# Performance work log

Hardware: AMD Instinct MI355X
Metric: run time of the kernel (lower is better)

## Reference

```python
import jax, jax.numpy as jnp
from jax import lax
import numpy as np

B, N, NPOINT, NSAMPLE, C = 4, 8192, 2048, 32, 128
RADIUS = 0.2
H1, H2, OUT = 64, 128, 128  # mlp: (3+C)->H1->H2, sas: H2->OUT


def fps(xyz, npoint):
    # furthest point sampling: xyz (B,N,3) -> idx (B,npoint) int32
    b, n, _ = xyz.shape
    init_idx = jnp.zeros((b,), jnp.int32)

    def step(carry, _):
        dist, last = carry
        p = jnp.take_along_axis(xyz, last[:, None, None], axis=1)  # (B,1,3)
        d = jnp.sum((xyz - p) ** 2, axis=-1)                       # (B,N)
        dist = jnp.minimum(dist, d)
        nxt = jnp.argmax(dist, axis=-1).astype(jnp.int32)
        return (dist, nxt), nxt

    (_, _), rest = lax.scan(step, (jnp.full((b, n), 1e10, jnp.float32), init_idx),
                            None, length=npoint - 1)
    return jnp.concatenate([init_idx[None, :], rest], axis=0).T    # (B,npoint)


def ball_query(xyz, new_xyz, radius, nsample):
    # xyz (B,N,3), new_xyz (B,S,3) -> idx (B,S,nsample) int32
    n = xyz.shape[1]
    d2 = jnp.sum((new_xyz[:, :, None, :] - xyz[:, None, :, :]) ** 2, axis=-1)  # (B,S,N)
    ar = jnp.arange(n, dtype=jnp.int32)
    keys = jnp.where(d2 <= radius * radius, ar, n)  # valid -> own index, invalid -> N
    neg_vals, _ = lax.top_k(-keys, nsample)          # smallest nsample keys
    idx = -neg_vals
    first = idx[..., :1]
    return jnp.where(idx >= n, first, idx)           # pad invalid with first valid


def gather_points(pts, idx):
    # pts (B,N,D), idx (B,S,ns) -> (B,S,ns,D)
    b, s, ns = idx.shape
    flat = jnp.take_along_axis(pts, idx.reshape(b, s * ns, 1), axis=1)
    return flat.reshape(b, s, ns, -1)


def setup_inputs() -> dict:
    key = jax.random.key(0)
    ks = jax.random.split(key, 8)
    xyz = jax.random.uniform(ks[0], (B, N, 3), dtype=jnp.float32)
    features = jax.random.normal(ks[1], (B, C, N), dtype=jnp.float32)
    cin = C + 3
    W1 = jax.random.normal(ks[2], (H1, cin), dtype=jnp.float32) / np.sqrt(cin)
    b1 = jnp.zeros((H1,), jnp.float32)
    W2 = jax.random.normal(ks[3], (H2, H1), dtype=jnp.float32) / np.sqrt(H1)
    b2 = jnp.zeros((H2,), jnp.float32)
    Wsa = jax.random.normal(ks[4], (OUT, H2), dtype=jnp.float32) / np.sqrt(H2)
    bsa = jnp.zeros((OUT,), jnp.float32)
    return {"xyz": xyz, "features": features, "W1": W1, "b1": b1,
            "W2": W2, "b2": b2, "Wsa": Wsa, "bsa": bsa}


def reference(xyz, features, W1, b1, W2, b2, Wsa, bsa):
    center_idx = fps(xyz, NPOINT)                                   # (B,S)
    new_xyz = jnp.take_along_axis(xyz, center_idx[:, :, None], axis=1)  # (B,S,3)
    g_idx = ball_query(xyz, new_xyz, RADIUS, NSAMPLE)               # (B,S,ns)
    g_xyz = gather_points(xyz, g_idx) - new_xyz[:, :, None, :]      # (B,S,ns,3) relative coords
    g_feat = gather_points(features.transpose(0, 2, 1), g_idx)      # (B,S,ns,C)
    h = jnp.concatenate([g_xyz, g_feat], axis=-1)                   # (B,S,ns,3+C)
    h = jax.nn.relu(jnp.einsum('bsnc,oc->bsno', h, W1) + b1)        # shared 1x1-conv MLP
    h = jax.nn.relu(jnp.einsum('bsnc,oc->bsno', h, W2) + b2)
    pooled = jnp.max(h, axis=2)                                     # max over nsample -> (B,S,H2)
    out = jnp.einsum('bsc,oc->bso', pooled, Wsa) + bsa              # sas channel mixer
    return new_xyz, out.transpose(0, 2, 1)                          # (B,S,3), (B,OUT,S)
```

## Files before the change

kernel.cpp:

```cpp
#include <hip/hip_runtime.h>
#include <cstdint>
#include <cstddef>

#define NB 4
#define NN 8192
#define NPTS 2048
#define NSAMP 32
#define NC 128
#define CIN 131
#define NH1 64
#define NH2 128
#define NOUTC 128
#define GCELLS 4096

typedef float v2f __attribute__((ext_vector_type(2)));
typedef unsigned long long ull;

__device__ __forceinline__ float d2_exact(float ax, float ay, float az,
                                          float bx, float by, float bz) {
  float dx = ax - bx, dy = ay - by, dz = az - bz;
  return __fadd_rn(__fadd_rn(__fmul_rn(dx, dx), __fmul_rn(dy, dy)),
                   __fmul_rn(dz, dz));
}

#if __has_builtin(__builtin_amdgcn_mov_dpp)
template <int CTRL>
__device__ __forceinline__ float dppf(float v) {
  return __int_as_float(
      __builtin_amdgcn_mov_dpp(__float_as_int(v), CTRL, 0xF, 0xF, true));
}
template <int CTRL>
__device__ __forceinline__ int dppi(int v) {
  return __builtin_amdgcn_mov_dpp(v, CTRL, 0xF, 0xF, true);
}
#else
template <int CTRL>
__device__ __forceinline__ float dppf(float v) {
  const int m = (CTRL == 0xB1) ? 1 : (CTRL == 0x4E) ? 2 : (CTRL == 0x141) ? 7 : 15;
  return __shfl_xor(v, m);
}
template <int CTRL>
__device__ __forceinline__ int dppi(int v) {
  const int m = (CTRL == 0xB1) ? 1 : (CTRL == 0x4E) ? 2 : (CTRL == 0x141) ? 7 : 15;
  return __shfl_xor(v, m);
}
#endif

template <int CTRL>
__device__ __forceinline__ ull dppk(ull k) {
  int hi = dppi<CTRL>((int)(k >> 32));
  int lo = dppi<CTRL>((int)(unsigned)k);
  return ((ull)(unsigned)hi << 32) | (unsigned)lo;
}
__device__ __forceinline__ ull shflk(ull k, int m) {
  int hi = __shfl_xor((int)(k >> 32), m);
  int lo = __shfl_xor((int)(unsigned)k, m);
  return ((ull)(unsigned)hi << 32) | (unsigned)lo;
}

template <int CTRL>
__device__ __forceinline__ void redk5(ull& k, float& x, float& y, float& z) {
  ull ok = dppk<CTRL>(k);
  float ox = dppf<CTRL>(x), oy = dppf<CTRL>(y), oz = dppf<CTRL>(z);
  bool t = ok > k;
  k = t ? ok : k;
  x = t ? ox : x;
  y = t ? oy : y;
  z = t ? oz : z;
}

__device__ __forceinline__ void red_pair(float& bv, int& bi, float ov, int oi) {
  bool t = (ov > bv) || (ov == bv && oi < bi);
  bv = t ? ov : bv;
  bi = t ? oi : bi;
}

#define SEL8V(A, kk, out)                     \
  {                                           \
    v2f t0_ = ((kk) & 2) ? A[1] : A[0];       \
    v2f t1_ = ((kk) & 2) ? A[3] : A[2];       \
    v2f t2_ = ((kk) & 4) ? t1_ : t0_;         \
    out = ((kk) & 1) ? t2_.y : t2_.x;         \
  }

__device__ __forceinline__ int spread3(int v) {
  return (v & 1) | ((v & 2) << 2) | ((v & 4) << 4) | ((v & 8) << 6);
}

__global__ __launch_bounds__(1024, 1) void sort_kernel(
    const float* __restrict__ xyz, float* __restrict__ xs,
    float* __restrict__ ys, float* __restrict__ zs, int* __restrict__ io) {
  __shared__ int hist[GCELLS];
  __shared__ int cbase[GCELLS];
  __shared__ int wtot[16];
  __shared__ int woff[16];
  const int b = blockIdx.x;
  const int tid = threadIdx.x;
  const int lane = tid & 63;
  const int wid = tid >> 6;
  const float* xb = xyz + (size_t)b * NN * 3;
  for (int i = tid; i < GCELLS; i += 1024) hist[i] = 0;
  __syncthreads();
  int cell[8];
  float px[8], py[8], pz[8];
#pragma unroll
  for (int k = 0; k < 8; ++k) {
    int j = tid + (k << 10);
    float x = xb[j * 3 + 0], y = xb[j * 3 + 1], z = xb[j * 3 + 2];
    px[k] = x; py[k] = y; pz[k] = z;
    int cx = min(15, max(0, (int)(x * 16.0f)));
    int cy = min(15, max(0, (int)(y * 16.0f)));
    int cz = min(15, max(0, (int)(z * 16.0f)));
    cell[k] = spread3(cx) | (spread3(cy) << 1) | (spread3(cz) << 2);
    atomicAdd(&hist[cell[k]], 1);
  }
  __syncthreads();
  const int i0 = tid * 4;
  int h0 = hist[i0], h1 = hist[i0 + 1], h2 = hist[i0 + 2], h3 = hist[i0 + 3];
  int s4 = h0 + h1 + h2 + h3;
  int v = s4;
#pragma unroll
  for (int d = 1; d < 64; d <<= 1) {
    int o = __shfl_up(v, d);
    if (lane >= d) v += o;
  }
  if (lane == 63) wtot[wid] = v;
  __syncthreads();
  if (tid < 16) {
    int acc = 0;
    for (int w = 0; w < 16; ++w) {
      if (w == tid) woff[tid] = acc;
      acc += wtot[w];
    }
  }
  __syncthreads();
  int eb = woff[wid] + v - s4;
  cbase[i0] = eb;
  cbase[i0 + 1] = eb + h0;
  cbase[i0 + 2] = eb + h0 + h1;
  cbase[i0 + 3] = eb + h0 + h1 + h2;
  __syncthreads();
  for (int i = tid; i < GCELLS; i += 1024) hist[i] = 0;
  __syncthreads();
  const size_t bo = (size_t)b * NN;
#pragma unroll
  for (int k = 0; k < 8; ++k) {
    int pos = cbase[cell[k]] + atomicAdd(&hist[cell[k]], 1);
    xs[bo + pos] = px[k];
    ys[bo + pos] = py[k];
    zs[bo + pos] = pz[k];
    io[bo + pos] = tid + (k << 10);
  }
}

__global__ __launch_bounds__(1024, 1) void fps_kernel(
    const float* __restrict__ xyz, const float* __restrict__ xs,
    const float* __restrict__ ys, const float* __restrict__ zs,
    const int* __restrict__ io, float* __restrict__ newxyz) {
#pragma clang fp contract(off)
  const int b = blockIdx.x;
  const int tid = threadIdx.x;
  const int lane = tid & 63;
  const int wid = tid >> 6;
  const size_t bo = (size_t)b * NN;

  v2f X2[4], Y2[4], Z2[4], D2[4];
  unsigned invI[8];
#pragma unroll
  for (int p = 0; p < 4; ++p) {
    int s0 = tid * 8 + 2 * p, s1 = s0 + 1;
    X2[p].x = xs[bo + s0]; X2[p].y = xs[bo + s1];
    Y2[p].x = ys[bo + s0]; Y2[p].y = ys[bo + s1];
    Z2[p].x = zs[bo + s0]; Z2[p].y = zs[bo + s1];
    invI[2 * p] = ~(unsigned)io[bo + s0];
    invI[2 * p + 1] = ~(unsigned)io[bo + s1];
    D2[p].x = 1e30f;
    D2[p].y = 1e30f;
  }

  __shared__ int skh[2][16], skl[2][16];
  __shared__ float sx[2][16], sy[2][16], sz[2][16];

  const float* xb = xyz + (size_t)b * NN * 3;
  float cx = xb[0], cy = xb[1], cz = xb[2];
  if (tid == 0) {
    newxyz[(size_t)b * NPTS * 3 + 0] = cx;
    newxyz[(size_t)b * NPTS * 3 + 1] = cy;
    newxyz[(size_t)b * NPTS * 3 + 2] = cz;
  }

  for (int t = 1; t < NPTS; ++t) {
    const int par = t & 1;
    const v2f cxv = {cx, cx}, cyv = {cy, cy}, czv = {cz, cz};
    ull bkey = 0ull;
    int kw = 0;
#pragma unroll
    for (int p = 0; p < 4; ++p) {
      v2f dx = X2[p] - cxv;
      v2f dy = Y2[p] - cyv;
      v2f dz = Z2[p] - czv;
      v2f s = dx * dx + dy * dy + dz * dz;
      v2f nd;
      nd.x = fminf(D2[p].x, s.x);
      nd.y = fminf(D2[p].y, s.y);
      D2[p] = nd;
      ull k0 = ((ull)__float_as_uint(nd.x) << 32) | invI[2 * p];
      bool c0 = k0 > bkey;
      bkey = c0 ? k0 : bkey;
      kw = c0 ? (2 * p) : kw;
      ull k1 = ((ull)__float_as_uint(nd.y) << 32) | invI[2 * p + 1];
      bool c1 = k1 > bkey;
      bkey = c1 ? k1 : bkey;
      kw = c1 ? (2 * p + 1) : kw;
    }
    ull rk = bkey;
    { ull o = dppk<0xB1>(rk);  rk = o > rk ? o : rk; }
    { ull o = dppk<0x4E>(rk);  rk = o > rk ? o : rk; }
    { ull o = dppk<0x141>(rk); rk = o > rk ? o : rk; }
    { ull o = dppk<0x140>(rk); rk = o > rk ? o : rk; }
    { ull o = shflk(rk, 16);   rk = o > rk ? o : rk; }
    { ull o = shflk(rk, 32);   rk = o > rk ? o : rk; }
    if (bkey == rk) {
      float ox, oy, oz;
      SEL8V(X2, kw, ox);
      SEL8V(Y2, kw, oy);
      SEL8V(Z2, kw, oz);
      skh[par][wid] = (int)(rk >> 32);
      skl[par][wid] = (int)(unsigned)rk;
      sx[par][wid] = ox;
      sy[par][wid] = oy;
      sz[par][wid] = oz;
    }
    __syncthreads();
    const int sl = lane & 15;
    ull mk = ((ull)(unsigned)skh[par][sl] << 32) | (unsigned)skl[par][sl];
    float xx = sx[par][sl], yy = sy[par][sl], zz = sz[par][sl];
    redk5<0xB1>(mk, xx, yy, zz);
    redk5<0x4E>(mk, xx, yy, zz);
    redk5<0x141>(mk, xx, yy, zz);
    redk5<0x140>(mk, xx, yy, zz);
    cx = xx;
    cy = yy;
    cz = zz;
    if (tid == 0) {
      size_t o = ((size_t)b * NPTS + t) * 3;
      newxyz[o + 0] = xx;
      newxyz[o + 1] = yy;
      newxyz[o + 2] = zz;
    }
  }
}

__global__ __launch_bounds__(1024, 1) void fps_nosort_kernel(
    const float* __restrict__ xyz, float* __restrict__ newxyz) {
#pragma clang fp contract(off)
  const int b = blockIdx.x;
  const int tid = threadIdx.x;
  const int lane = tid & 63;
  const int wid = tid >> 6;
  const float* xb = xyz + (size_t)b * NN * 3;
  v2f x2[4], y2[4], z2[4], dd[4];
#pragma unroll
  for (int p = 0; p < 4; ++p) {
    int j0 = tid + ((2 * p) << 10);
    int j1 = tid + ((2 * p + 1) << 10);
    x2[p].x = xb[j0 * 3 + 0]; x2[p].y = xb[j1 * 3 + 0];
    y2[p].x = xb[j0 * 3 + 1]; y2[p].y = xb[j1 * 3 + 1];
    z2[p].x = xb[j0 * 3 + 2]; z2[p].y = xb[j1 * 3 + 2];
    dd[p].x = 1e10f; dd[p].y = 1e10f;
  }
  __shared__ float vbuf[2][16];
  __shared__ int ibuf[2][16];
  __shared__ float cbuf[2][16][3];
  float cx = xb[0], cy = xb[1], cz = xb[2];
  if (tid == 0) {
    newxyz[(size_t)b * NPTS * 3 + 0] = cx;
    newxyz[(size_t)b * NPTS * 3 + 1] = cy;
    newxyz[(size_t)b * NPTS * 3 + 2] = cz;
  }
  for (int t = 1; t < NPTS; ++t) {
    const int par = t & 1;
    float bv = -1.0f; int bi = 0;
    float bwx = 0.f, bwy = 0.f, bwz = 0.f;
#pragma unroll
    for (int p = 0; p < 4; ++p) {
      v2f dx = x2[p] - (v2f){cx, cx};
      v2f dy = y2[p] - (v2f){cy, cy};
      v2f dz = z2[p] - (v2f){cz, cz};
      v2f s = dx * dx + dy * dy + dz * dz;
      v2f nd;
      nd.x = fminf(dd[p].x, s.x);
      nd.y = fminf(dd[p].y, s.y);
      dd[p] = nd;
      { bool c = nd.x > bv;
        bv = c ? nd.x : bv; bi = c ? (tid + ((2 * p) << 10)) : bi;
        bwx = c ? x2[p].x : bwx; bwy = c ? y2[p].x : bwy; bwz = c ? z2[p].x : bwz; }
      { bool c = nd.y > bv;
        bv = c ? nd.y : bv; bi = c ? (tid + ((2 * p + 1) << 10)) : bi;
        bwx = c ? x2[p].y : bwx; bwy = c ? y2[p].y : bwy; bwz = c ? z2[p].y : bwz; }
    }
    red_pair(bv, bi, dppf<0xB1>(bv), dppi<0xB1>(bi));
    red_pair(bv, bi, dppf<0x4E>(bv), dppi<0x4E>(bi));
    red_pair(bv, bi, dppf<0x141>(bv), dppi<0x141>(bi));
    red_pair(bv, bi, dppf<0x140>(bv), dppi<0x140>(bi));
    red_pair(bv, bi, __shfl_xor(bv, 16), __shfl_xor(bi, 16));
    red_pair(bv, bi, __shfl_xor(bv, 32), __shfl_xor(bi, 32));
    if (tid == (bi & 1023)) {
      vbuf[par][wid] = bv; ibuf[par][wid] = bi;
      cbuf[par][wid][0] = bwx; cbuf[par][wid][1] = bwy; cbuf[par][wid][2] = bwz;
    }
    __syncthreads();
    float v2w = vbuf[par][lane & 15];
    int i2w = ibuf[par][lane & 15];
    red_pair(v2w, i2w, dppf<0xB1>(v2w), dppi<0xB1>(i2w));
    red_pair(v2w, i2w, dppf<0x4E>(v2w), dppi<0x4E>(i2w));
    red_pair(v2w, i2w, dppf<0x141>(v2w), dppi<0x141>(i2w));
    red_pair(v2w, i2w, dppf<0x140>(v2w), dppi<0x140>(i2w));
    const int slot = (i2w & 1023) >> 6;
    cx = cbuf[par][slot][0]; cy = cbuf[par][slot][1]; cz = cbuf[par][slot][2];
    if (tid == (i2w & 1023)) {
      size_t o = ((size_t)b * NPTS + t) * 3;
      newxyz[o + 0] = cx; newxyz[o + 1] = cy; newxyz[o + 2] = cz;
    }
  }
}

__global__ __launch_bounds__(256) void ballq_kernel(
    const float* __restrict__ xyz, const float* __restrict__ newxyz,
    int* __restrict__ bidx) {
  const int cid = blockIdx.x * 4 + (threadIdx.x >> 6);
  const int lane = threadIdx.x & 63;
  const int b = cid >> 11;
  const float* xb = xyz + (size_t)b * NN * 3;
  const float cx = newxyz[(size_t)cid * 3 + 0];
  const float cy = newxyz[(size_t)cid * 3 + 1];
  const float cz = newxyz[(size_t)cid * 3 + 2];
  int* ob = bidx + (size_t)cid * NSAMP;
  int total = 0;
  int first = -1;
  for (int c0 = 0; c0 < NN; c0 += 64) {
    int j = c0 + lane;
    float xx = xb[j * 3 + 0], yy = xb[j * 3 + 1], zz = xb[j * 3 + 2];
    float d2 = d2_exact(cx, cy, cz, xx, yy, zz);
    bool in = d2 <= 0.04f;
    unsigned long long m = __ballot(in);
    if (first < 0 && m) first = c0 + __builtin_ctzll(m);
    int pos = total + __popcll(m & ((1ull << lane) - 1ull));
    if (in && pos < NSAMP) ob[pos] = j;
    total += __popcll(m);
    if (total >= NSAMP) break;
  }
  if (total < NSAMP && lane < NSAMP - total) ob[total + lane] = first;
}

__global__ void tw_kernel(const float* __restrict__ W1, const float* __restrict__ W2,
                          const float* __restrict__ Wsa, float* __restrict__ w1t,
                          float* __restrict__ w2t, float* __restrict__ wsat) {
  int i = blockIdx.x * blockDim.x + threadIdx.x;
  if (i < CIN * NH1) w1t[i] = W1[(i % NH1) * CIN + (i / NH1)];
  if (i < NH1 * NH2) w2t[i] = W2[(i % NH2) * NH1 + (i / NH2)];
  if (i < NH2 * NOUTC) wsat[i] = Wsa[(i % NOUTC) * NH2 + (i / NOUTC)];
}

__global__ void tfeat_kernel(const float* __restrict__ feat, float* __restrict__ featT) {
  __shared__ float tile[32][33];
  const int b = blockIdx.z;
  const int n0 = blockIdx.x * 32, c0 = blockIdx.y * 32;
  const int tx = threadIdx.x, ty = threadIdx.y;
#pragma unroll
  for (int r = 0; r < 4; ++r)
    tile[ty + r * 8][tx] = feat[((size_t)b * NC + c0 + ty + r * 8) * NN + n0 + tx];
  __syncthreads();
#pragma unroll
  for (int r = 0; r < 4; ++r)
    featT[((size_t)b * NN + n0 + ty + r * 8) * NC + c0 + tx] = tile[tx][ty + r * 8];
}

#define HS 36
__global__ __launch_bounds__(256) void mlp_kernel(
    const float* __restrict__ xyz, const float* __restrict__ fsrc,
    const float* __restrict__ newxyz, const int* __restrict__ bidx,
    const float* __restrict__ w1t, const float* __restrict__ b1,
    const float* __restrict__ w2t, const float* __restrict__ b2,
    const float* __restrict__ wsat, const float* __restrict__ bsa,
    float* __restrict__ out1, int useT) {
  __shared__ float h[CIN * HS];
  __shared__ float h1[NH1 * HS];
  __shared__ float pl[256];
  __shared__ float pooled[NH2];
  __shared__ int sidx[NSAMP];
  __shared__ float sc[3];
  const int cid = blockIdx.x;
  const int b = cid >> 11;
  const int s = cid & 2047;
  const int tid = threadIdx.x;
  if (tid < NSAMP) sidx[tid] = bidx[(size_t)cid * NSAMP + tid];
  if (tid < 3) sc[tid] = newxyz[(size_t)cid * 3 + tid];
  __syncthreads();
  {
    const int ss = tid >> 3, q = tid & 7;
    const int j = sidx[ss];
    if (useT) {
      const float4* fr = (const float4*)(fsrc + ((size_t)b * NN + j) * NC + q * 16);
#pragma unroll
      for (int u = 0; u < 4; ++u) {
        float4 v = fr[u];
        int c = 3 + q * 16 + u * 4;
        h[(c + 0) * HS + ss] = v.x;
        h[(c + 1) * HS + ss] = v.y;
        h[(c + 2) * HS + ss] = v.z;
        h[(c + 3) * HS + ss] = v.w;
      }
    } else {
      for (int u = 0; u < 16; ++u) {
        int c = q * 16 + u;
        h[(3 + c) * HS + ss] = fsrc[((size_t)b * NC + c) * NN + j];
      }
    }
    if (q == 0) {
      const float* pr = xyz + ((size_t)b * NN + j) * 3;
      h[0 * HS + ss] = pr[0] - sc[0];
      h[1 * HS + ss] = pr[1] - sc[1];
      h[2 * HS + ss] = pr[2] - sc[2];
    }
  }
  __syncthreads();
  {
    const int o = tid & 63, sg = tid >> 6;
    float acc[8];
    const float bb = b1[o];
#pragma unroll
    for (int i = 0; i < 8; ++i) acc[i] = bb;
    const float4* hb = (const float4*)&h[sg * 8];
    for (int k = 0; k < CIN; ++k) {
      float w = w1t[k * NH1 + o];
      float4 a = hb[k * (HS / 4) + 0];
      float4 c = hb[k * (HS / 4) + 1];
      acc[0] = fmaf(w, a.x, acc[0]); acc[1] = fmaf(w, a.y, acc[1]);
      acc[2] = fmaf(w, a.z, acc[2]); acc[3] = fmaf(w, a.w, acc[3]);
      acc[4] = fmaf(w, c.x, acc[4]); acc[5] = fmaf(w, c.y, acc[5]);
      acc[6] = fmaf(w, c.z, acc[6]); acc[7] = fmaf(w, c.w, acc[7]);
    }
#pragma unroll
    for (int i = 0; i < 8; ++i) h1[o * HS + sg * 8 + i] = fmaxf(acc[i], 0.0f);
  }
  __syncthreads();
  {
    const int o = tid & 127, sg = tid >> 7;
    float acc[16];
    const float bb = b2[o];
#pragma unroll
    for (int i = 0; i < 16; ++i) acc[i] = bb;
    const float4* hb = (const float4*)&h1[sg * 16];
    for (int k = 0; k < NH1; ++k) {
      float w = w2t[k * NH2 + o];
#pragma unroll
      for (int u = 0; u < 4; ++u) {
        float4 a = hb[k * (HS / 4) + u];
        acc[u * 4 + 0] = fmaf(w, a.x, acc[u * 4 + 0]);
        acc[u * 4 + 1] = fmaf(w, a.y, acc[u * 4 + 1]);
        acc[u * 4 + 2] = fmaf(w, a.z, acc[u * 4 + 2]);
        acc[u * 4 + 3] = fmaf(w, a.w, acc[u * 4 + 3]);
      }
    }
    float pm = acc[0];
#pragma unroll
    for (int i = 1; i < 16; ++i) pm = fmaxf(pm, acc[i]);
    pl[sg * 128 + o] = pm;
  }
  __syncthreads();
  if (tid < NH2) pooled[tid] = fmaxf(fmaxf(pl[tid], pl[128 + tid]), 0.0f);
  __syncthreads();
  if (tid < NOUTC) {
    float acc = bsa[tid];
    for (int k = 0; k < NH2; ++k) acc = fmaf(pooled[k], wsat[k * NOUTC + tid], acc);
    out1[((size_t)b * NOUTC + tid) * NPTS + s] = acc;
  }
}

extern "C" void kernel_launch(void* const* d_in, const int* in_sizes, int n_in,
                              void* d_out, int out_size, void* d_ws, size_t ws_size,
                              hipStream_t stream) {
  const float* xyz = (const float*)d_in[0];
  const float* feat = (const float*)d_in[1];
  const float* W1 = (const float*)d_in[2];
  const float* b1 = (const float*)d_in[3];
  const float* W2 = (const float*)d_in[4];
  const float* b2 = (const float*)d_in[5];
  const float* Wsa = (const float*)d_in[6];
  const float* bsa = (const float*)d_in[7];
  float* out = (float*)d_out;
  float* newxyz = out;
  float* out1 = out + (size_t)NB * NPTS * 3;

  const size_t sort_f = (size_t)NB * NN * 4;
  const size_t small_f = (size_t)CIN * NH1 + NH1 * NH2 + NH2 * NOUTC +
                         (size_t)NB * NPTS * NSAMP;
  const size_t featT_f = (size_t)NB * NN * NC;

  float* ws = (float*)d_ws;
  bool useSort = ws_size >= (sort_f + small_f) * 4;
  bool useT = ws_size >= (sort_f + small_f + featT_f) * 4;

  float* xs = ws;
  float* ysr = xs + (size_t)NB * NN;
  float* zsr = ysr + (size_t)NB * NN;
  int* iosr = (int*)(zsr + (size_t)NB * NN);
  float* base2 = useSort ? (ws + sort_f) : ws;
  float* w1t = base2;
  float* w2t = w1t + CIN * NH1;
  float* wsat = w2t + NH1 * NH2;
  int* bidx = (int*)(wsat + NH2 * NOUTC);
  float* featT = (float*)(bidx + (size_t)NB * NPTS * NSAMP);

  tw_kernel<<<64, 256, 0, stream>>>(W1, W2, Wsa, w1t, w2t, wsat);
  if (useT)
    tfeat_kernel<<<dim3(NN / 32, NC / 32, NB), dim3(32, 8), 0, stream>>>(feat, featT);
  if (useSort) {
    sort_kernel<<<NB, 1024, 0, stream>>>(xyz, xs, ysr, zsr, iosr);
    fps_kernel<<<NB, 1024, 0, stream>>>(xyz, xs, ysr, zsr, iosr, newxyz);
  } else {
    fps_nosort_kernel<<<NB, 1024, 0, stream>>>(xyz, newxyz);
  }
  ballq_kernel<<<NB * NPTS / 4, 256, 0, stream>>>(xyz, newxyz, bidx);
  mlp_kernel<<<NB * NPTS, 256, 0, stream>>>(xyz, useT ? featT : feat, newxyz, bidx,
                                            w1t, b1, w2t, b2, wsat, bsa, out1,
                                            (int)useT);
}
```

Before: 3.679 ms.

## Halve FPS block size to 512 threads with 16 points per thread

The FPS kernel now runs 512 threads per batch block, each holding 16 sorted points in scalar registers instead of 8 in packed float2 vectors. This halves the number of waves taking part in each iteration's barrier and cross-wave reduction, so the shared-memory argmax drops one DPP step. In exchange, each thread does twice the serial distance and key-compare work per step, uses a deeper 16-way select, and gives up the packed float2 arithmetic.

```diff
diff --git a/kernel.cpp b/kernel.cpp
--- a/kernel.cpp
+++ b/kernel.cpp
@@ -75,12 +75,23 @@
   bi = t ? oi : bi;
 }
 
-#define SEL8V(A, kk, out)                     \
-  {                                           \
-    v2f t0_ = ((kk) & 2) ? A[1] : A[0];       \
-    v2f t1_ = ((kk) & 2) ? A[3] : A[2];       \
-    v2f t2_ = ((kk) & 4) ? t1_ : t0_;         \
-    out = ((kk) & 1) ? t2_.y : t2_.x;         \
+#define SEL16(A, kk, out)                                              \
+  {                                                                    \
+    float a0_ = ((kk) & 1) ? A[1] : A[0];                              \
+    float a1_ = ((kk) & 1) ? A[3] : A[2];                              \
+    float a2_ = ((kk) & 1) ? A[5] : A[4];                              \
+    float a3_ = ((kk) & 1) ? A[7] : A[6];                              \
+    float a4_ = ((kk) & 1) ? A[9] : A[8];                              \
+    float a5_ = ((kk) & 1) ? A[11] : A[10];                            \
+    float a6_ = ((kk) & 1) ? A[13] : A[12];                            \
+    float a7_ = ((kk) & 1) ? A[15] : A[14];                            \
+    float b0_ = ((kk) & 2) ? a1_ : a0_;                                \
+    float b1_ = ((kk) & 2) ? a3_ : a2_;                                \
+    float b2_ = ((kk) & 2) ? a5_ : a4_;                                \
+    float b3_ = ((kk) & 2) ? a7_ : a6_;                                \
+    float c0_ = ((kk) & 4) ? b1_ : b0_;                                \
+    float c1_ = ((kk) & 4) ? b3_ : b2_;                                \
+    out = ((kk) & 8) ? c1_ : c0_;                                      \
   }
 
 __device__ __forceinline__ int spread3(int v) {
@@ -153,7 +164,7 @@
   }
 }
 
-__global__ __launch_bounds__(1024, 1) void fps_kernel(
+__global__ __launch_bounds__(512, 1) void fps_kernel(
     const float* __restrict__ xyz, const float* __restrict__ xs,
     const float* __restrict__ ys, const float* __restrict__ zs,
     const int* __restrict__ io, float* __restrict__ newxyz) {
@@ -164,22 +175,20 @@
   const int wid = tid >> 6;
   const size_t bo = (size_t)b * NN;
 
-  v2f X2[4], Y2[4], Z2[4], D2[4];
-  unsigned invI[8];
-#pragma unroll
-  for (int p = 0; p < 4; ++p) {
-    int s0 = tid * 8 + 2 * p, s1 = s0 + 1;
-    X2[p].x = xs[bo + s0]; X2[p].y = xs[bo + s1];
-    Y2[p].x = ys[bo + s0]; Y2[p].y = ys[bo + s1];
-    Z2[p].x = zs[bo + s0]; Z2[p].y = zs[bo + s1];
-    invI[2 * p] = ~(unsigned)io[bo + s0];
-    invI[2 * p + 1] = ~(unsigned)io[bo + s1];
-    D2[p].x = 1e30f;
-    D2[p].y = 1e30f;
-  }
-
-  __shared__ int skh[2][16], skl[2][16];
-  __shared__ float sx[2][16], sy[2][16], sz[2][16];
+  float X[16], Y[16], Z[16], D[16];
+  unsigned invI[16];
+#pragma unroll
+  for (int k = 0; k < 16; ++k) {
+    int s = tid * 16 + k;
+    X[k] = xs[bo + s];
+    Y[k] = ys[bo + s];
+    Z[k] = zs[bo + s];
+    invI[k] = ~(unsigned)io[bo + s];
+    D[k] = 1e30f;
+  }
+
+  __shared__ int skh[2][8], skl[2][8];
+  __shared__ float sx[2][8], sy[2][8], sz[2][8];
 
   const float* xb = xyz + (size_t)b * NN * 3;
   float cx = xb[0], cy = xb[1], cz = xb[2];
@@ -191,27 +200,21 @@
 
   for (int t = 1; t < NPTS; ++t) {
     const int par = t & 1;
-    const v2f cxv = {cx, cx}, cyv = {cy, cy}, czv = {cz, cz};
     ull bkey = 0ull;
     int kw = 0;
 #pragma unroll
-    for (int p = 0; p < 4; ++p) {
-      v2f dx = X2[p] - cxv;
-      v2f dy = Y2[p] - cyv;
-      v2f dz = Z2[p] - czv;
-      v2f s = dx * dx + dy * dy + dz * dz;
-      v2f nd;
-      nd.x = fminf(D2[p].x, s.x);
-      nd.y = fminf(D2[p].y, s.y);
-      D2[p] = nd;
-      ull k0 = ((ull)__float_as_uint(nd.x) << 32) | invI[2 * p];
-      bool c0 = k0 > bkey;
-      bkey = c0 ? k0 : bkey;
-      kw = c0 ? (2 * p) : kw;
-      ull k1 = ((ull)__float_as_uint(nd.y) << 32) | invI[2 * p + 1];
-      bool c1 = k1 > bkey;
-      bkey = c1 ? k1 : bkey;
-      kw = c1 ? (2 * p + 1) : kw;
+    for (int k = 0; k < 16; ++k) {
+      float dx = X[k] - cx;
+      float dy = Y[k] - cy;
+      float dz = Z[k] - cz;
+      float s = __fadd_rn(__fadd_rn(__fmul_rn(dx, dx), __fmul_rn(dy, dy)),
+                          __fmul_rn(dz, dz));
+      float nd = fminf(D[k], s);
+      D[k] = nd;
+      ull key = ((ull)__float_as_uint(nd) << 32) | invI[k];
+      bool c = key > bkey;
+      bkey = c ? key : bkey;
+      kw = c ? k : kw;
     }
     ull rk = bkey;
     { ull o = dppk<0xB1>(rk);  rk = o > rk ? o : rk; }
@@ -222,9 +225,9 @@
     { ull o = shflk(rk, 32);   rk = o > rk ? o : rk; }
     if (bkey == rk) {
       float ox, oy, oz;
-      SEL8V(X2, kw, ox);
-      SEL8V(Y2, kw, oy);
-      SEL8V(Z2, kw, oz);
+      SEL16(X, kw, ox);
+      SEL16(Y, kw, oy);
+      SEL16(Z, kw, oz);
       skh[par][wid] = (int)(rk >> 32);
       skl[par][wid] = (int)(unsigned)rk;
       sx[par][wid] = ox;
@@ -232,13 +235,12 @@
       sz[par][wid] = oz;
     }
     __syncthreads();
-    const int sl = lane & 15;
+    const int sl = lane & 7;
     ull mk = ((ull)(unsigned)skh[par][sl] << 32) | (unsigned)skl[par][sl];
     float xx = sx[par][sl], yy = sy[par][sl], zz = sz[par][sl];
     redk5<0xB1>(mk, xx, yy, zz);
     redk5<0x4E>(mk, xx, yy, zz);
     redk5<0x141>(mk, xx, yy, zz);
-    redk5<0x140>(mk, xx, yy, zz);
     cx = xx;
     cy = yy;
     cz = zz;
@@ -518,7 +520,7 @@
     tfeat_kernel<<<dim3(NN / 32, NC / 32, NB), dim3(32, 8), 0, stream>>>(feat, featT);
   if (useSort) {
     sort_kernel<<<NB, 1024, 0, stream>>>(xyz, xs, ysr, zsr, iosr);
-    fps_kernel<<<NB, 1024, 0, stream>>>(xyz, xs, ysr, zsr, iosr, newxyz);
+    fps_kernel<<<NB, 512, 0, stream>>>(xyz, xs, ysr, zsr, iosr, newxyz);
   } else {
     fps_nosort_kernel<<<NB, 1024, 0, stream>>>(xyz, newxyz);
   }
```

New measurement: 3.662 ms. About the same (-0.5%).
